# Optimization experiments

Measured on AMD Instinct MI355X. Metric: run time of the kernel, lower is better.

Reference implementation:

```python
import jax, jax.numpy as jnp
import numpy as np

K_NEIGS = 3
M_PROB = 1.0
EPS = 1e-12


def _gen_G_single(ft):
    """Build normalized hypergraph Laplacian G [N,N] from node coords ft [N,3].

    Mirrors construct_H_with_KNN (is_probH=True, m_prob=1) + generate_G_from_H
    from the HGNN reference code: per-center KNN hyperedges with probabilistic
    incidence exp(-d^2/(m_prob*avg_d)^2), then G = Dv^-1/2 H De^-1 H^T Dv^-1/2.
    """
    N = ft.shape[0]
    # squared pairwise Euclidean distances [N,N]
    sq_norm = jnp.sum(ft * ft, axis=1)
    sq = jnp.maximum(sq_norm[:, None] + sq_norm[None, :] - 2.0 * ft @ ft.T, 0.0)
    dist = jnp.sqrt(sq + EPS)
    avg_dis = jnp.mean(dist, axis=1)  # per-center mean distance [N]
    # K nearest neighbors per center (self is always included: sq[c,c]=0)
    neg_sq, idx = jax.lax.top_k(-sq, K_NEIGS)  # [N,K]
    # prob incidence: exp(-d^2 / (m_prob*avg)^2); neg_sq = -d^2
    vals = jnp.exp(neg_sq / (M_PROB * avg_dis[:, None]) ** 2)  # [N,K]
    # H[node, edge]: column c holds the K neighbors of center c
    H = jnp.zeros((N, N), ft.dtype).at[idx, jnp.arange(N)[:, None]].set(vals)
    de = jnp.sum(H, axis=0)              # edge degrees [N]
    dv = jnp.sum(H, axis=1)              # vertex degrees [N]
    inv_de = 1.0 / de
    dv2 = dv ** -0.5
    HW = H * inv_de[None, :]
    G = (dv2[:, None] * (HW @ H.T)) * dv2[None, :]
    return G


def reference(x, W1, b1, Wc, bc):
    # gen_G: per-batch hypergraph G [B,N,N]
    G = jax.vmap(_gen_G_single)(x)
    # HGNN_conv with both args = G: out = G @ (G @ W1 + b1)  -> [B,N,H1]
    f = jnp.matmul(G, jnp.matmul(G, W1) + b1)
    # max-pool over nodes, then classifier
    f = jnp.max(f, axis=1)               # [B,H1]
    return f @ Wc + bc                   # [B,class_num]


def setup_inputs() -> dict:
    key = jax.random.key(0)
    k1, k2, k3, k4, k5 = jax.random.split(key, 5)
    B, N, H1, C = 4, 2048, 128, 8
    x = jax.random.normal(k1, (B, N, 3), dtype=jnp.float32)
    W1 = jax.random.normal(k2, (N, H1), dtype=jnp.float32) / np.sqrt(N)
    b1 = jax.random.normal(k3, (H1,), dtype=jnp.float32) * 0.01
    Wc = jax.random.normal(k4, (H1, C), dtype=jnp.float32) / np.sqrt(H1)
    bc = jax.random.normal(k5, (C,), dtype=jnp.float32) * 0.01
    return {"x": x, "W1": W1, "b1": b1, "Wc": Wc, "bc": bc}
```

## Files before the change

### kernel.cpp

```cpp
#include <hip/hip_runtime.h>
#include <math.h>

#define NN 2048
#define BB 4
#define HD 128
#define CNUM 8
#define WPB 4
#define PCHUNK 64
#define NCHUNKS (NN / PCHUNK)

typedef unsigned long long u64;

__device__ __forceinline__ u64 pack_key(float sq, int j) {
    return ((u64)__float_as_uint(sq) << 32) | (unsigned)j;
}
__device__ __forceinline__ void ins3(u64 k, u64& k0, u64& k1, u64& k2) {
    u64 a = k  < k2 ? k  : k2;
    u64 b = k0 > a  ? k0 : a;
    k0    = k0 < a  ? k0 : a;
    k2    = k1 > b  ? k1 : b;
    k1    = k1 < b  ? k1 : b;
}

__global__ void k_prep(const float* __restrict__ x, float4* __restrict__ pts) {
    const int t = blockIdx.x * 256 + threadIdx.x;
    const float a = x[3 * t], c = x[3 * t + 1], d = x[3 * t + 2];
    pts[t] = make_float4(a, c, d, a * a + c * c + d * d);
}

__global__ __launch_bounds__(256) void k_dist(
        const float4* __restrict__ pts,
        int* __restrict__ idx, float* __restrict__ vals,
        float* __restrict__ de, float* __restrict__ dv) {
    const int b = blockIdx.y;
    const float4* pb = pts + b * NN;
    const int wave = threadIdx.x >> 6;
    const int lane = threadIdx.x & 63;
    const int i = blockIdx.x * WPB + wave;
    const float4 ci = pb[i];
    u64 k0 = ~0ull, k1 = ~0ull, k2 = ~0ull;
    float dsA = 0.f, dsB = 0.f;
    for (int t = lane; t < NN; t += 256) {
        const float4 pa = pb[t];
        const float4 pv = pb[t + 64];
        const float4 pc = pb[t + 128];
        const float4 pd = pb[t + 192];
        const float qa = fmaxf(ci.w + pa.w - 2.0f * (ci.x * pa.x + ci.y * pa.y + ci.z * pa.z), 0.0f);
        const float qb = fmaxf(ci.w + pv.w - 2.0f * (ci.x * pv.x + ci.y * pv.y + ci.z * pv.z), 0.0f);
        const float qc = fmaxf(ci.w + pc.w - 2.0f * (ci.x * pc.x + ci.y * pc.y + ci.z * pc.z), 0.0f);
        const float qd = fmaxf(ci.w + pd.w - 2.0f * (ci.x * pd.x + ci.y * pd.y + ci.z * pd.z), 0.0f);
        dsA += __builtin_amdgcn_sqrtf(qa + 1e-12f) + __builtin_amdgcn_sqrtf(qc + 1e-12f);
        dsB += __builtin_amdgcn_sqrtf(qb + 1e-12f) + __builtin_amdgcn_sqrtf(qd + 1e-12f);
        ins3(pack_key(qa, t),       k0, k1, k2);
        ins3(pack_key(qb, t + 64),  k0, k1, k2);
        ins3(pack_key(qc, t + 128), k0, k1, k2);
        ins3(pack_key(qd, t + 192), k0, k1, k2);
    }
    float dsum = dsA + dsB;
    for (int off = 32; off > 0; off >>= 1) {
        const u64 o0 = __shfl_xor(k0, off);
        const u64 o1 = __shfl_xor(k1, off);
        const u64 o2 = __shfl_xor(k2, off);
        dsum += __shfl_xor(dsum, off);
        ins3(o0, k0, k1, k2);
        ins3(o1, k0, k1, k2);
        ins3(o2, k0, k1, k2);
    }
    if (lane == 0) {
        const float s0 = __uint_as_float((unsigned)(k0 >> 32));
        const float s1 = __uint_as_float((unsigned)(k1 >> 32));
        const float s2 = __uint_as_float((unsigned)(k2 >> 32));
        const int   i0 = (int)(k0 & 0xffffffffu);
        const int   i1 = (int)(k1 & 0xffffffffu);
        const int   i2 = (int)(k2 & 0xffffffffu);
        const float avg = dsum * (1.0f / NN);
        const float inva2 = 1.0f / (avg * avg);
        const float v0 = expf(-s0 * inva2);
        const float v1 = expf(-s1 * inva2);
        const float v2 = expf(-s2 * inva2);
        const int base = (b * NN + i) * 3;
        idx[base] = i0; idx[base + 1] = i1; idx[base + 2] = i2;
        vals[base] = v0; vals[base + 1] = v1; vals[base + 2] = v2;
        de[b * NN + i] = v0 + v1 + v2;
        atomicAdd(&dv[b * NN + i0], v0);
        atomicAdd(&dv[b * NN + i1], v1);
        atomicAdd(&dv[b * NN + i2], v2);
    }
}

__global__ void k_conv1(const float* __restrict__ W1, const int* __restrict__ idx,
                        const float* __restrict__ vals, const float* __restrict__ de,
                        const float* __restrict__ dv, float* __restrict__ Z1) {
    const int e = blockIdx.x * 2 + (threadIdx.x >> 7);
    const int b = blockIdx.y, h = threadIdx.x & (HD - 1);
    const int base = (b * NN + e) * 3;
    const int j0 = idx[base], j1 = idx[base + 1], j2 = idx[base + 2];
    const float v0 = vals[base], v1 = vals[base + 1], v2 = vals[base + 2];
    const float ide = 1.0f / de[b * NN + e];
    const float g0 = v0 * rsqrtf(dv[b * NN + j0]);
    const float g1 = v1 * rsqrtf(dv[b * NN + j1]);
    const float g2 = v2 * rsqrtf(dv[b * NN + j2]);
    const float y = ide * (g0 * W1[j0 * HD + h] + g1 * W1[j1 * HD + h] + g2 * W1[j2 * HD + h]);
    atomicAdd(&Z1[((size_t)(b * NN + j0)) * HD + h], v0 * y);
    atomicAdd(&Z1[((size_t)(b * NN + j1)) * HD + h], v1 * y);
    atomicAdd(&Z1[((size_t)(b * NN + j2)) * HD + h], v2 * y);
}

__global__ void k_conv2(const float* __restrict__ b1, const int* __restrict__ idx,
                        const float* __restrict__ vals, const float* __restrict__ de,
                        const float* __restrict__ dv, const float* __restrict__ Z1,
                        float* __restrict__ Z2) {
    const int e = blockIdx.x * 2 + (threadIdx.x >> 7);
    const int b = blockIdx.y, h = threadIdx.x & (HD - 1);
    const int base = (b * NN + e) * 3;
    const int j0 = idx[base], j1 = idx[base + 1], j2 = idx[base + 2];
    const float v0 = vals[base], v1 = vals[base + 1], v2 = vals[base + 2];
    const float ide = 1.0f / de[b * NN + e];
    const float bh = b1[h];
    const float d0 = rsqrtf(dv[b * NN + j0]);
    const float d1 = rsqrtf(dv[b * NN + j1]);
    const float d2 = rsqrtf(dv[b * NN + j2]);
    const float f0 = d0 * Z1[((size_t)(b * NN + j0)) * HD + h] + bh;
    const float f1 = d1 * Z1[((size_t)(b * NN + j1)) * HD + h] + bh;
    const float f2 = d2 * Z1[((size_t)(b * NN + j2)) * HD + h] + bh;
    const float y = ide * (v0 * d0 * f0 + v1 * d1 * f1 + v2 * d2 * f2);
    atomicAdd(&Z2[((size_t)(b * NN + j0)) * HD + h], v0 * y);
    atomicAdd(&Z2[((size_t)(b * NN + j1)) * HD + h], v1 * y);
    atomicAdd(&Z2[((size_t)(b * NN + j2)) * HD + h], v2 * y);
}

__global__ void k_pool1(const float* __restrict__ dv, const float* __restrict__ Z2,
                        float* __restrict__ pmax) {
    const int b = blockIdx.x, ch = blockIdx.y, h = threadIdx.x;
    const int v0 = ch * PCHUNK;
    float mx = -INFINITY;
    for (int v = v0; v < v0 + PCHUNK; ++v) {
        const float d2 = rsqrtf(dv[b * NN + v]);
        mx = fmaxf(mx, d2 * Z2[((size_t)(b * NN + v)) * HD + h]);
    }
    pmax[(b * NCHUNKS + ch) * HD + h] = mx;
}

__global__ void k_pool2(const float* __restrict__ Wc, const float* __restrict__ bc,
                        const float* __restrict__ pmax, float* __restrict__ out) {
    __shared__ float smax[HD];
    const int b = blockIdx.x, h = threadIdx.x;
    float mx = -INFINITY;
    for (int c = 0; c < NCHUNKS; ++c)
        mx = fmaxf(mx, pmax[(b * NCHUNKS + c) * HD + h]);
    smax[h] = mx;
    __syncthreads();
    if (h < CNUM) {
        float acc = bc[h];
        for (int q = 0; q < HD; ++q) acc += smax[q] * Wc[q * CNUM + h];
        out[b * CNUM + h] = acc;
    }
}

extern "C" void kernel_launch(void* const* d_in, const int* in_sizes, int n_in,
                              void* d_out, int out_size, void* d_ws, size_t ws_size,
                              hipStream_t stream) {
    const float* x  = (const float*)d_in[0];
    const float* W1 = (const float*)d_in[1];
    const float* b1 = (const float*)d_in[2];
    const float* Wc = (const float*)d_in[3];
    const float* bc = (const float*)d_in[4];
    float* out = (float*)d_out;

    float* ws = (float*)d_ws;
    float* dv   = ws;
    float* Z1   = dv + BB * NN;
    float* Z2   = Z1 + (size_t)BB * NN * HD;
    float* vals = Z2 + (size_t)BB * NN * HD;
    float* de   = vals + BB * NN * 3;
    int*   idx  = (int*)(de + BB * NN);
    float* pmax = (float*)(idx + BB * NN * 3);
    float4* pts = (float4*)(pmax + BB * NCHUNKS * HD);

    hipMemsetAsync(dv, 0, (size_t)(BB * NN) * (1 + 2 * HD) * sizeof(float), stream);

    k_prep<<<BB * NN / 256, 256, 0, stream>>>(x, pts);
    k_dist<<<dim3(NN / WPB, BB), 256, 0, stream>>>(pts, idx, vals, de, dv);
    k_conv1<<<dim3(NN / 2, BB), 256, 0, stream>>>(W1, idx, vals, de, dv, Z1);
    k_conv2<<<dim3(NN / 2, BB), 256, 0, stream>>>(b1, idx, vals, de, dv, Z1, Z2);
    k_pool1<<<dim3(BB, NCHUNKS), HD, 0, stream>>>(dv, Z2, pmax);
    k_pool2<<<BB, HD, 0, stream>>>(Wc, bc, pmax, out);
}
```

Measured before the change: 119.7 us.

## Replace atomic scatter convolutions with reverse-index gather and fuse pooling

Builds a per-node reverse adjacency list (capped at 64 entries) during the KNN kernel, so both convolution passes gather through it instead of scattering with float atomics into large zeroed buffers. The second convolution also computes the max-pool directly, which removes the separate pool kernel and the large Z buffers along with their memset. Point preprocessing moves into shared memory inside the distance kernel, so the prep kernel is gone. In exchange, every block redundantly loads all points into LDS, and any node referenced by more than 64 hyperedges would be silently truncated.

Measured after the change: 139.8 us. +16.8%, slower.

```diff
diff --git a/kernel.cpp b/kernel.cpp
--- a/kernel.cpp
+++ b/kernel.cpp
@@ -6,8 +6,9 @@
 #define HD 128
 #define CNUM 8
 #define WPB 4
-#define PCHUNK 64
-#define NCHUNKS (NN / PCHUNK)
+#define CAP 64
+#define NPB 8
+#define NCH (NN / NPB)
 
 typedef unsigned long long u64;
 
@@ -22,29 +23,31 @@
     k1    = k1 < b  ? k1 : b;
 }
 
-__global__ void k_prep(const float* __restrict__ x, float4* __restrict__ pts) {
-    const int t = blockIdx.x * 256 + threadIdx.x;
-    const float a = x[3 * t], c = x[3 * t + 1], d = x[3 * t + 2];
-    pts[t] = make_float4(a, c, d, a * a + c * c + d * d);
-}
-
 __global__ __launch_bounds__(256) void k_dist(
-        const float4* __restrict__ pts,
+        const float* __restrict__ x,
         int* __restrict__ idx, float* __restrict__ vals,
-        float* __restrict__ de, float* __restrict__ dv) {
+        float* __restrict__ de, float* __restrict__ dv,
+        int* __restrict__ cnt, int2* __restrict__ rev) {
+    __shared__ float4 sp[NN];
     const int b = blockIdx.y;
-    const float4* pb = pts + b * NN;
+    const float* xb = x + (size_t)b * NN * 3;
+    for (int q = threadIdx.x; q < NN; q += 256) {
+        const float a = xb[3 * q], c = xb[3 * q + 1], d = xb[3 * q + 2];
+        sp[q] = make_float4(a, c, d, a * a + c * c + d * d);
+    }
+    __syncthreads();
+
     const int wave = threadIdx.x >> 6;
     const int lane = threadIdx.x & 63;
     const int i = blockIdx.x * WPB + wave;
-    const float4 ci = pb[i];
+    const float4 ci = sp[i];
     u64 k0 = ~0ull, k1 = ~0ull, k2 = ~0ull;
     float dsA = 0.f, dsB = 0.f;
     for (int t = lane; t < NN; t += 256) {
-        const float4 pa = pb[t];
-        const float4 pv = pb[t + 64];
-        const float4 pc = pb[t + 128];
-        const float4 pd = pb[t + 192];
+        const float4 pa = sp[t];
+        const float4 pv = sp[t + 64];
+        const float4 pc = sp[t + 128];
+        const float4 pd = sp[t + 192];
         const float qa = fmaxf(ci.w + pa.w - 2.0f * (ci.x * pa.x + ci.y * pa.y + ci.z * pa.z), 0.0f);
         const float qb = fmaxf(ci.w + pv.w - 2.0f * (ci.x * pv.x + ci.y * pv.y + ci.z * pv.z), 0.0f);
         const float qc = fmaxf(ci.w + pc.w - 2.0f * (ci.x * pc.x + ci.y * pc.y + ci.z * pc.z), 0.0f);
@@ -85,75 +88,100 @@
         atomicAdd(&dv[b * NN + i0], v0);
         atomicAdd(&dv[b * NN + i1], v1);
         atomicAdd(&dv[b * NN + i2], v2);
-    }
-}
-
-__global__ void k_conv1(const float* __restrict__ W1, const int* __restrict__ idx,
-                        const float* __restrict__ vals, const float* __restrict__ de,
-                        const float* __restrict__ dv, float* __restrict__ Z1) {
-    const int e = blockIdx.x * 2 + (threadIdx.x >> 7);
-    const int b = blockIdx.y, h = threadIdx.x & (HD - 1);
-    const int base = (b * NN + e) * 3;
-    const int j0 = idx[base], j1 = idx[base + 1], j2 = idx[base + 2];
-    const float v0 = vals[base], v1 = vals[base + 1], v2 = vals[base + 2];
-    const float ide = 1.0f / de[b * NN + e];
-    const float g0 = v0 * rsqrtf(dv[b * NN + j0]);
-    const float g1 = v1 * rsqrtf(dv[b * NN + j1]);
-    const float g2 = v2 * rsqrtf(dv[b * NN + j2]);
-    const float y = ide * (g0 * W1[j0 * HD + h] + g1 * W1[j1 * HD + h] + g2 * W1[j2 * HD + h]);
-    atomicAdd(&Z1[((size_t)(b * NN + j0)) * HD + h], v0 * y);
-    atomicAdd(&Z1[((size_t)(b * NN + j1)) * HD + h], v1 * y);
-    atomicAdd(&Z1[((size_t)(b * NN + j2)) * HD + h], v2 * y);
-}
-
-__global__ void k_conv2(const float* __restrict__ b1, const int* __restrict__ idx,
-                        const float* __restrict__ vals, const float* __restrict__ de,
-                        const float* __restrict__ dv, const float* __restrict__ Z1,
-                        float* __restrict__ Z2) {
-    const int e = blockIdx.x * 2 + (threadIdx.x >> 7);
-    const int b = blockIdx.y, h = threadIdx.x & (HD - 1);
-    const int base = (b * NN + e) * 3;
-    const int j0 = idx[base], j1 = idx[base + 1], j2 = idx[base + 2];
-    const float v0 = vals[base], v1 = vals[base + 1], v2 = vals[base + 2];
-    const float ide = 1.0f / de[b * NN + e];
-    const float bh = b1[h];
-    const float d0 = rsqrtf(dv[b * NN + j0]);
-    const float d1 = rsqrtf(dv[b * NN + j1]);
-    const float d2 = rsqrtf(dv[b * NN + j2]);
-    const float f0 = d0 * Z1[((size_t)(b * NN + j0)) * HD + h] + bh;
-    const float f1 = d1 * Z1[((size_t)(b * NN + j1)) * HD + h] + bh;
-    const float f2 = d2 * Z1[((size_t)(b * NN + j2)) * HD + h] + bh;
-    const float y = ide * (v0 * d0 * f0 + v1 * d1 * f1 + v2 * d2 * f2);
-    atomicAdd(&Z2[((size_t)(b * NN + j0)) * HD + h], v0 * y);
-    atomicAdd(&Z2[((size_t)(b * NN + j1)) * HD + h], v1 * y);
-    atomicAdd(&Z2[((size_t)(b * NN + j2)) * HD + h], v2 * y);
-}
-
-__global__ void k_pool1(const float* __restrict__ dv, const float* __restrict__ Z2,
-                        float* __restrict__ pmax) {
-    const int b = blockIdx.x, ch = blockIdx.y, h = threadIdx.x;
-    const int v0 = ch * PCHUNK;
+        const int p0 = atomicAdd(&cnt[b * NN + i0], 1);
+        if (p0 < CAP) rev[((size_t)(b * NN + i0)) * CAP + p0] = make_int2(i, __float_as_int(v0));
+        const int p1 = atomicAdd(&cnt[b * NN + i1], 1);
+        if (p1 < CAP) rev[((size_t)(b * NN + i1)) * CAP + p1] = make_int2(i, __float_as_int(v1));
+        const int p2 = atomicAdd(&cnt[b * NN + i2], 1);
+        if (p2 < CAP) rev[((size_t)(b * NN + i2)) * CAP + p2] = make_int2(i, __float_as_int(v2));
+    }
+}
+
+__global__ __launch_bounds__(256) void k_conv1(
+        const float* __restrict__ W1, const float* __restrict__ b1,
+        const int* __restrict__ idx, const float* __restrict__ vals,
+        const float* __restrict__ de, const float* __restrict__ dv,
+        const int* __restrict__ cnt, const int2* __restrict__ rev,
+        float* __restrict__ f1) {
+    const int b = blockIdx.y;
+    const int i = blockIdx.x * 2 + (threadIdx.x >> 7);
+    const int h = threadIdx.x & (HD - 1);
+    const int ni = b * NN + i;
+    const int cn = min(cnt[ni], CAP);
+    float acc = 0.f;
+    for (int s = 0; s < cn; ++s) {
+        const int2 r = rev[(size_t)ni * CAP + s];
+        const int e = r.x;
+        const float v = __int_as_float(r.y);
+        const int eb = (b * NN + e) * 3;
+        const int j0 = idx[eb], j1 = idx[eb + 1], j2 = idx[eb + 2];
+        const float v0 = vals[eb], v1 = vals[eb + 1], v2 = vals[eb + 2];
+        const float ide = 1.0f / de[b * NN + e];
+        const float g0 = v0 * rsqrtf(dv[b * NN + j0]);
+        const float g1 = v1 * rsqrtf(dv[b * NN + j1]);
+        const float g2 = v2 * rsqrtf(dv[b * NN + j2]);
+        const float y = ide * (g0 * W1[j0 * HD + h] + g1 * W1[j1 * HD + h] + g2 * W1[j2 * HD + h]);
+        acc += v * y;
+    }
+    f1[(size_t)ni * HD + h] = rsqrtf(dv[ni]) * acc + b1[h];
+}
+
+__global__ __launch_bounds__(256) void k_conv2(
+        const int* __restrict__ idx, const float* __restrict__ vals,
+        const float* __restrict__ de, const float* __restrict__ dv,
+        const int* __restrict__ cnt, const int2* __restrict__ rev,
+        const float* __restrict__ f1, float* __restrict__ pmax) {
+    __shared__ float smx[2][HD];
+    const int b = blockIdx.y;
+    const int sub = threadIdx.x >> 7;
+    const int h = threadIdx.x & (HD - 1);
     float mx = -INFINITY;
-    for (int v = v0; v < v0 + PCHUNK; ++v) {
-        const float d2 = rsqrtf(dv[b * NN + v]);
-        mx = fmaxf(mx, d2 * Z2[((size_t)(b * NN + v)) * HD + h]);
-    }
-    pmax[(b * NCHUNKS + ch) * HD + h] = mx;
+    for (int t = 0; t < NPB / 2; ++t) {
+        const int i = blockIdx.x * NPB + t * 2 + sub;
+        const int ni = b * NN + i;
+        const int cn = min(cnt[ni], CAP);
+        float acc = 0.f;
+        for (int s = 0; s < cn; ++s) {
+            const int2 r = rev[(size_t)ni * CAP + s];
+            const int e = r.x;
+            const float v = __int_as_float(r.y);
+            const int eb = (b * NN + e) * 3;
+            const int j0 = idx[eb], j1 = idx[eb + 1], j2 = idx[eb + 2];
+            const float v0 = vals[eb], v1 = vals[eb + 1], v2 = vals[eb + 2];
+            const float ide = 1.0f / de[b * NN + e];
+            const float g0 = v0 * rsqrtf(dv[b * NN + j0]);
+            const float g1 = v1 * rsqrtf(dv[b * NN + j1]);
+            const float g2 = v2 * rsqrtf(dv[b * NN + j2]);
+            const float y = ide * (g0 * f1[((size_t)(b * NN + j0)) * HD + h]
+                                 + g1 * f1[((size_t)(b * NN + j1)) * HD + h]
+                                 + g2 * f1[((size_t)(b * NN + j2)) * HD + h]);
+            acc += v * y;
+        }
+        mx = fmaxf(mx, rsqrtf(dv[ni]) * acc);
+    }
+    smx[sub][h] = mx;
+    __syncthreads();
+    if (sub == 0)
+        pmax[((size_t)b * NCH + blockIdx.x) * HD + h] = fmaxf(smx[0][h], smx[1][h]);
 }
 
 __global__ void k_pool2(const float* __restrict__ Wc, const float* __restrict__ bc,
                         const float* __restrict__ pmax, float* __restrict__ out) {
-    __shared__ float smax[HD];
-    const int b = blockIdx.x, h = threadIdx.x;
+    __shared__ float s2[2][HD];
+    const int b = blockIdx.x;
+    const int h = threadIdx.x & (HD - 1);
+    const int half = threadIdx.x >> 7;
     float mx = -INFINITY;
-    for (int c = 0; c < NCHUNKS; ++c)
-        mx = fmaxf(mx, pmax[(b * NCHUNKS + c) * HD + h]);
-    smax[h] = mx;
-    __syncthreads();
-    if (h < CNUM) {
-        float acc = bc[h];
-        for (int q = 0; q < HD; ++q) acc += smax[q] * Wc[q * CNUM + h];
-        out[b * CNUM + h] = acc;
+    for (int c = half; c < NCH; c += 2)
+        mx = fmaxf(mx, pmax[((size_t)b * NCH + c) * HD + h]);
+    s2[half][h] = mx;
+    __syncthreads();
+    if (half == 0) s2[0][h] = fmaxf(s2[0][h], s2[1][h]);
+    __syncthreads();
+    if (threadIdx.x < CNUM) {
+        float acc = bc[threadIdx.x];
+        for (int q = 0; q < HD; ++q) acc += s2[0][q] * Wc[q * CNUM + threadIdx.x];
+        out[b * CNUM + threadIdx.x] = acc;
     }
 }
 
@@ -169,20 +197,18 @@
 
     float* ws = (float*)d_ws;
     float* dv   = ws;
-    float* Z1   = dv + BB * NN;
-    float* Z2   = Z1 + (size_t)BB * NN * HD;
-    float* vals = Z2 + (size_t)BB * NN * HD;
-    float* de   = vals + BB * NN * 3;
+    int*   cnt  = (int*)(dv + BB * NN);
+    float* de   = (float*)(cnt + BB * NN);
     int*   idx  = (int*)(de + BB * NN);
-    float* pmax = (float*)(idx + BB * NN * 3);
-    float4* pts = (float4*)(pmax + BB * NCHUNKS * HD);
-
-    hipMemsetAsync(dv, 0, (size_t)(BB * NN) * (1 + 2 * HD) * sizeof(float), stream);
-
-    k_prep<<<BB * NN / 256, 256, 0, stream>>>(x, pts);
-    k_dist<<<dim3(NN / WPB, BB), 256, 0, stream>>>(pts, idx, vals, de, dv);
-    k_conv1<<<dim3(NN / 2, BB), 256, 0, stream>>>(W1, idx, vals, de, dv, Z1);
-    k_conv2<<<dim3(NN / 2, BB), 256, 0, stream>>>(b1, idx, vals, de, dv, Z1, Z2);
-    k_pool1<<<dim3(BB, NCHUNKS), HD, 0, stream>>>(dv, Z2, pmax);
-    k_pool2<<<BB, HD, 0, stream>>>(Wc, bc, pmax, out);
-}
+    float* vals = (float*)(idx + BB * NN * 3);
+    int2*  rev  = (int2*)(vals + BB * NN * 3);
+    float* f1   = (float*)(rev + (size_t)BB * NN * CAP);
+    float* pmax = f1 + (size_t)BB * NN * HD;
+
+    hipMemsetAsync(dv, 0, (size_t)2 * BB * NN * sizeof(float), stream);
+
+    k_dist <<<dim3(NN / WPB, BB), 256, 0, stream>>>(x, idx, vals, de, dv, cnt, rev);
+    k_conv1<<<dim3(NN / 2,  BB), 256, 0, stream>>>(W1, b1, idx, vals, de, dv, cnt, rev, f1);
+    k_conv2<<<dim3(NN / NPB, BB), 256, 0, stream>>>(idx, vals, de, dv, cnt, rev, f1, pmax);
+    k_pool2<<<BB, 256, 0, stream>>>(Wc, bc, pmax, out);
+}
```
